# Optimization experiments

Measured on AMD Instinct MI355X. Metric: run time of the kernel, lower is better.

## Reference

```python
import jax, jax.numpy as jnp
import numpy as np

N, D, H, O, E, K = 8192, 1024, 4096, 1024, 8, 3  # tokens, in_dim, hidden, out_dim, experts, topk


def setup_inputs() -> dict:
    key = jax.random.key(0)
    ks = jax.random.split(key, 4)
    s = 0.02
    return {
        "x": jax.random.normal(ks[0], (N, D), jnp.float32),
        "gate_w": jax.random.normal(ks[1], (D, E), jnp.float32) * s,
        "gate_b": jnp.zeros((E,), jnp.float32),
        "w1": jax.random.normal(ks[2], (E, D, H), jnp.float32) * s,
        "b1": jnp.zeros((E, H), jnp.float32),
        "w2": jax.random.normal(ks[3], (E, H, O), jnp.float32) * s,
        "b2": jnp.zeros((E, O), jnp.float32),
    }


def reference(x, gate_w, gate_b, w1, b1, w2, b2):
    # Gate: scores over experts, top-k mask, softmax renormalized over selected experts
    scores = x @ gate_w + gate_b                                   # [N, E]
    _, topk_idx = jax.lax.top_k(scores, K)                         # [N, K]
    mask = jax.nn.one_hot(topk_idx, E, dtype=scores.dtype).sum(1)  # [N, E] (topk indices are distinct)
    weights = jax.nn.softmax(scores, axis=-1) * mask
    weights = weights / (weights.sum(-1, keepdims=True) + 1e-8)
    # Dense all-expert MLP (faithful to original: every expert runs on every token)
    h = jax.nn.relu(jnp.einsum('nd,edh->neh', x, w1) + b1)         # [N, E, H]
    outs = jnp.einsum('neh,eho->neo', h, w2) + b2                  # [N, E, O]
    # Weighted combine over experts
    return jnp.einsum('ne,neo->no', weights, outs)                 # [N, O]
```

## Files before the change

### kernel.cpp

```cpp
#include <hip/hip_runtime.h>
#include <hip/hip_bf16.h>
#include <hip/hip_fp16.h>

#define N_TOK 8192
#define DIM_D 1024
#define DIM_H 4096
#define DIM_O 1024
#define NEXP  8
#define TOPK  3

#define CAP_ROWS  25600
#define MAX_TILES 200
#define NXCD      8
#define MT_PER    (MAX_TILES / NXCD)
#define MT_GRP    5

typedef _Float16 f16_t;
typedef _Float16 f16x4 __attribute__((ext_vector_type(4)));
typedef _Float16 f16x8 __attribute__((ext_vector_type(8)));
typedef float    floatx4 __attribute__((ext_vector_type(4)));

__device__ __forceinline__ void gld_lds16(const void* g, void* l) {
  __builtin_amdgcn_global_load_lds(
      (__attribute__((address_space(1))) void*)(void*)g,
      (__attribute__((address_space(3))) void*)l, 16, 0, 0);
}

__device__ __forceinline__ void decode_tile(int bid, int nbn, int* mt, int* nidx) {
  const int xcd = bid & (NXCD - 1);
  const int lid = bid >> 3;
  const int per = MT_GRP * nbn;
  const int group = lid / per;
  const int rem = lid - group * per;
  const int n = rem / MT_GRP;
  const int g = rem - n * MT_GRP;
  *mt = xcd * MT_PER + group * MT_GRP + g;
  *nidx = n;
}

__global__ __launch_bounds__(256) void gate_kernel(
    const float* __restrict__ x, const float* __restrict__ gw,
    const float* __restrict__ gb, float* __restrict__ wts,
    int* __restrict__ lists, int* __restrict__ cnt) {
  const int token = blockIdx.x * 4 + (threadIdx.x >> 6);
  const int lane = threadIdx.x & 63;
  float s[NEXP];
#pragma unroll
  for (int e = 0; e < NEXP; e++) s[e] = 0.f;
  const float* xr = x + (size_t)token * DIM_D;
  for (int d = lane; d < DIM_D; d += 64) {
    const float xv = xr[d];
    const float* g = gw + (size_t)d * NEXP;
#pragma unroll
    for (int e = 0; e < NEXP; e++) s[e] += xv * g[e];
  }
#pragma unroll
  for (int off = 32; off > 0; off >>= 1) {
#pragma unroll
    for (int e = 0; e < NEXP; e++) s[e] += __shfl_xor(s[e], off, 64);
  }
#pragma unroll
  for (int e = 0; e < NEXP; e++) s[e] += gb[e];

  float mx = s[0];
#pragma unroll
  for (int e = 1; e < NEXP; e++) mx = fmaxf(mx, s[e]);
  float p[NEXP];
  float den = 0.f;
#pragma unroll
  for (int e = 0; e < NEXP; e++) { p[e] = expf(s[e] - mx); den += p[e]; }

  bool sel[NEXP];
#pragma unroll
  for (int e = 0; e < NEXP; e++) sel[e] = false;
  for (int k = 0; k < TOPK; k++) {
    int bj = 0;
    float bv = -1e30f;
#pragma unroll
    for (int e = 0; e < NEXP; e++) {
      if (!sel[e] && s[e] > bv) { bv = s[e]; bj = e; }
    }
    sel[bj] = true;
  }
  float msum = 1e-8f * den;
#pragma unroll
  for (int e = 0; e < NEXP; e++) msum += sel[e] ? p[e] : 0.f;
  const float inv = 1.f / msum;
  if (lane < NEXP) {
    wts[(size_t)token * NEXP + lane] = sel[lane] ? p[lane] * inv : 0.f;
  }
  if (lane == 0) {
#pragma unroll
    for (int e = 0; e < NEXP; e++) {
      if (sel[e]) {
        const int pos = atomicAdd(&cnt[e], 1);
        lists[e * N_TOK + pos] = token;
      }
    }
  }
}

__global__ void plan_kernel(const int* __restrict__ cnt, int* __restrict__ start,
                            int* __restrict__ table, int* __restrict__ total) {
  if (threadIdx.x == 0) {
    int r0 = 0, t = 0;
    for (int e = 0; e < NEXP; e++) {
      start[e] = r0;
      const int nt = (cnt[e] + 127) >> 7;
      for (int i = 0; i < nt; i++) table[t++] = (e << 16) | ((r0 >> 7) + i);
      r0 += nt << 7;
    }
    total[0] = t;
  }
}

__global__ __launch_bounds__(256) void fill_kernel(
    const int* __restrict__ cnt, const int* __restrict__ start,
    const int* __restrict__ lists, const float* __restrict__ wts,
    int* __restrict__ rowtok, float* __restrict__ roww) {
  const int e = blockIdx.y;
  const int i = blockIdx.x * 256 + threadIdx.x;
  const int c = cnt[e];
  const int pad = (c + 127) & ~127;
  if (i >= pad) return;
  const int r = start[e] + i;
  if (i < c) {
    const int t = lists[e * N_TOK + i];
    rowtok[r] = t;
    roww[r] = wts[(size_t)t * NEXP + e];
  } else {
    rowtok[r] = -1;
    roww[r] = 0.f;
  }
}

__global__ __launch_bounds__(256) void cvt_f32_f16(
    const float* __restrict__ in, f16_t* __restrict__ out, int n4) {
  const int i = blockIdx.x * 256 + threadIdx.x;
  if (i >= n4) return;
  const float4 v = ((const float4*)in)[i];
  f16x4 o;
  o.x = (f16_t)v.x; o.y = (f16_t)v.y; o.z = (f16_t)v.z; o.w = (f16_t)v.w;
  ((f16x4*)out)[i] = o;
}

__global__ __launch_bounds__(256) void cvt_transpose(
    const float* __restrict__ in, f16_t* __restrict__ out, int R, int C) {
  __shared__ float tile[32][33];
  const int e = blockIdx.z;
  const int r0 = blockIdx.y * 32, c0 = blockIdx.x * 32;
  const int lc = threadIdx.x & 31, lr0 = threadIdx.x >> 5;
  const float* src = in + (size_t)e * R * C;
#pragma unroll
  for (int i = 0; i < 4; i++) {
    const int rr = lr0 + i * 8;
    tile[rr][lc] = src[(size_t)(r0 + rr) * C + c0 + lc];
  }
  __syncthreads();
  f16_t* dst = out + (size_t)e * C * R;
#pragma unroll
  for (int i = 0; i < 4; i++) {
    const int cc = lr0 + i * 8;
    dst[(size_t)(c0 + cc) * R + r0 + lc] = (f16_t)tile[lc][cc];
  }
}

__global__ __launch_bounds__(256, 2) void gemm1_moe(
    const f16_t* __restrict__ xb, const f16_t* __restrict__ w1t,
    const float* __restrict__ b1, const int* __restrict__ rowtok,
    const int* __restrict__ table, const int* __restrict__ total,
    f16_t* __restrict__ hg, int Hc, int cH, int nbn) {
  int mt, nidx;
  decode_tile(blockIdx.x, nbn, &mt, &nidx);
  if (mt >= total[0]) return;
  const int ent = table[mt];
  const int e = ent >> 16;
  const int r0 = (ent & 0xffff) << 7;
  const int n0 = nidx * 128;

  __shared__ __align__(16) f16_t Asm[128 * 32];
  __shared__ __align__(16) f16_t Bsm[128 * 32];
  const int tid = threadIdx.x;
  const int wave = tid >> 6, lane = tid & 63;
  const int q = lane >> 4, r = lane & 15;
  const int waveM = (wave >> 1) * 64, waveN = (wave & 1) * 64;

  const floatx4 zero = {0.f, 0.f, 0.f, 0.f};
  floatx4 acc[4][4];
#pragma unroll
  for (int mi = 0; mi < 4; mi++)
#pragma unroll
    for (int ni = 0; ni < 4; ni++) acc[mi][ni] = zero;

  const f16_t* BT = w1t + (size_t)e * DIM_H * DIM_D + (size_t)cH * DIM_D;

  const int s0 = tid, s1 = tid + 256;
  const int row0 = s0 >> 2, row1 = s1 >> 2;
  const int gs0 = (s0 & 3) ^ ((row0 >> 1) & 3);
  const int gs1 = (s1 & 3) ^ ((row1 >> 1) & 3);
  const int tok0 = max(rowtok[r0 + row0], 0);
  const int tok1 = max(rowtok[r0 + row1], 0);
  const f16_t* Ar0 = xb + (size_t)tok0 * DIM_D + gs0 * 8;
  const f16_t* Ar1 = xb + (size_t)tok1 * DIM_D + gs1 * 8;
  const f16_t* Br0 = BT + (size_t)(n0 + row0) * DIM_D + gs0 * 8;
  const f16_t* Br1 = BT + (size_t)(n0 + row1) * DIM_D + gs1 * 8;
  f16_t* AsmB0 = &Asm[(wave * 64) * 8];
  f16_t* AsmB1 = &Asm[(256 + wave * 64) * 8];
  f16_t* BsmB0 = &Bsm[(wave * 64) * 8];
  f16_t* BsmB1 = &Bsm[(256 + wave * 64) * 8];

  for (int k0 = 0; k0 < DIM_D; k0 += 32) {
    gld_lds16(Ar0 + k0, AsmB0);
    gld_lds16(Ar1 + k0, AsmB1);
    gld_lds16(Br0 + k0, BsmB0);
    gld_lds16(Br1 + k0, BsmB1);
    __syncthreads();
    f16x8 af[4], bfr[4];
#pragma unroll
    for (int i = 0; i < 4; i++) {
      const int rowa = waveM + i * 16 + r;
      af[i] = *(const f16x8*)&Asm[rowa * 32 + ((q ^ ((rowa >> 1) & 3)) << 3)];
      const int rowb = waveN + i * 16 + r;
      bfr[i] = *(const f16x8*)&Bsm[rowb * 32 + ((q ^ ((rowb >> 1) & 3)) << 3)];
    }
#pragma unroll
    for (int mi = 0; mi < 4; mi++)
#pragma unroll
      for (int ni = 0; ni < 4; ni++)
        acc[mi][ni] = __builtin_amdgcn_mfma_f32_16x16x32_f16(
            af[mi], bfr[ni], acc[mi][ni], 0, 0, 0);
    __syncthreads();
  }

#pragma unroll
  for (int mi = 0; mi < 4; mi++)
#pragma unroll
    for (int ni = 0; ni < 4; ni++) {
      const int gcol = n0 + waveN + ni * 16 + r;
      const float bv = b1[(size_t)e * DIM_H + cH + gcol];
#pragma unroll
      for (int rr = 0; rr < 4; rr++) {
        const int grow = r0 + waveM + mi * 16 + q * 4 + rr;
        hg[(size_t)grow * Hc + gcol] = (f16_t)fmaxf(acc[mi][ni][rr] + bv, 0.f);
      }
    }
}

__global__ __launch_bounds__(256, 2) void gemm2_moe(
    const f16_t* __restrict__ hg, const f16_t* __restrict__ w2t,
    const float* __restrict__ b2, const int* __restrict__ rowtok,
    const float* __restrict__ roww, const int* __restrict__ table,
    const int* __restrict__ total, float* __restrict__ out, int Hc, int cH,
    int addBias) {
  int mt, nidx;
  decode_tile(blockIdx.x, DIM_O / 128, &mt, &nidx);
  if (mt >= total[0]) return;
  const int ent = table[mt];
  const int e = ent >> 16;
  const int r0 = (ent & 0xffff) << 7;
  const int n0 = nidx * 128;

  __shared__ __align__(16) f16_t Asm[128 * 32];
  __shared__ __align__(16) f16_t Bsm[128 * 32];
  const int tid = threadIdx.x;
  const int wave = tid >> 6, lane = tid & 63;
  const int q = lane >> 4, r = lane & 15;
  const int waveM = (wave >> 1) * 64, waveN = (wave & 1) * 64;

  const floatx4 zero = {0.f, 0.f, 0.f, 0.f};
  floatx4 acc[4][4];
#pragma unroll
  for (int mi = 0; mi < 4; mi++)
#pragma unroll
    for (int ni = 0; ni < 4; ni++) acc[mi][ni] = zero;

  const f16_t* BT = w2t + (size_t)e * DIM_O * DIM_H + cH;

  const int s0 = tid, s1 = tid + 256;
  const int row0 = s0 >> 2, row1 = s1 >> 2;
  const int gs0 = (s0 & 3) ^ ((row0 >> 1) & 3);
  const int gs1 = (s1 & 3) ^ ((row1 >> 1) & 3);
  const f16_t* Ar0 = hg + (size_t)(r0 + row0) * Hc + gs0 * 8;
  const f16_t* Ar1 = hg + (size_t)(r0 + row1) * Hc + gs1 * 8;
  const f16_t* Br0 = BT + (size_t)(n0 + row0) * DIM_H + gs0 * 8;
  const f16_t* Br1 = BT + (size_t)(n0 + row1) * DIM_H + gs1 * 8;
  f16_t* AsmB0 = &Asm[(wave * 64) * 8];
  f16_t* AsmB1 = &Asm[(256 + wave * 64) * 8];
  f16_t* BsmB0 = &Bsm[(wave * 64) * 8];
  f16_t* BsmB1 = &Bsm[(256 + wave * 64) * 8];

  for (int k0 = 0; k0 < Hc; k0 += 32) {
    gld_lds16(Ar0 + k0, AsmB0);
    gld_lds16(Ar1 + k0, AsmB1);
    gld_lds16(Br0 + k0, BsmB0);
    gld_lds16(Br1 + k0, BsmB1);
    __syncthreads();
    f16x8 af[4], bfr[4];
#pragma unroll
    for (int i = 0; i < 4; i++) {
      const int rowa = waveM + i * 16 + r;
      af[i] = *(const f16x8*)&Asm[rowa * 32 + ((q ^ ((rowa >> 1) & 3)) << 3)];
      const int rowb = waveN + i * 16 + r;
      bfr[i] = *(const f16x8*)&Bsm[rowb * 32 + ((q ^ ((rowb >> 1) & 3)) << 3)];
    }
#pragma unroll
    for (int mi = 0; mi < 4; mi++)
#pragma unroll
      for (int ni = 0; ni < 4; ni++)
        acc[mi][ni] = __builtin_amdgcn_mfma_f32_16x16x32_f16(
            af[mi], bfr[ni], acc[mi][ni], 0, 0, 0);
    __syncthreads();
  }

#pragma unroll
  for (int mi = 0; mi < 4; mi++)
#pragma unroll
    for (int ni = 0; ni < 4; ni++) {
      const int gcol = n0 + waveN + ni * 16 + r;
      const float bv = addBias ? b2[(size_t)e * DIM_O + gcol] : 0.f;
#pragma unroll
      for (int rr = 0; rr < 4; rr++) {
        const int grow = r0 + waveM + mi * 16 + q * 4 + rr;
        const int t = rowtok[grow];
        if (t >= 0) {
          const float w = roww[grow];
          unsafeAtomicAdd(&out[(size_t)t * DIM_O + gcol],
                          w * (acc[mi][ni][rr] + bv));
        }
      }
    }
}

extern "C" void kernel_launch(void* const* d_in, const int* in_sizes, int n_in,
                              void* d_out, int out_size, void* d_ws, size_t ws_size,
                              hipStream_t stream) {
  const float* x      = (const float*)d_in[0];
  const float* gate_w = (const float*)d_in[1];
  const float* gate_b = (const float*)d_in[2];
  const float* w1     = (const float*)d_in[3];
  const float* b1     = (const float*)d_in[4];
  const float* w2     = (const float*)d_in[5];
  const float* b2     = (const float*)d_in[6];
  float* out = (float*)d_out;

  char* ws = (char*)d_ws;
  const size_t off_wts    = 0;
  const size_t off_lists  = off_wts + 262144;
  const size_t off_cnt    = off_lists + 262144;
  const size_t off_start  = off_cnt + 512;
  const size_t off_total  = off_start + 512;
  const size_t off_table  = off_total + 512;
  const size_t off_rowtok = off_table + 2048;
  const size_t off_roww   = off_rowtok + 102400;
  const size_t META       = 1 << 20;
  const size_t off_w1t = META;
  const size_t off_w2t = off_w1t + (size_t)NEXP * DIM_H * DIM_D * 2;
  const size_t off_xb  = off_w2t + (size_t)NEXP * DIM_O * DIM_H * 2;
  const size_t off_hg  = off_xb + (size_t)N_TOK * DIM_D * 2;

  float* wts   = (float*)(ws + off_wts);
  int*   lists = (int*)(ws + off_lists);
  int*   cnt   = (int*)(ws + off_cnt);
  int*   start = (int*)(ws + off_start);
  int*   total = (int*)(ws + off_total);
  int*   table = (int*)(ws + off_table);
  int*   rowtok= (int*)(ws + off_rowtok);
  float* roww  = (float*)(ws + off_roww);
  f16_t* w1t   = (f16_t*)(ws + off_w1t);
  f16_t* w2t   = (f16_t*)(ws + off_w2t);
  f16_t* xb    = (f16_t*)(ws + off_xb);
  f16_t* hg    = (f16_t*)(ws + off_hg);

  int Hc = 512;
  for (int cand = 4096; cand >= 512; cand >>= 1) {
    if (off_hg + (size_t)CAP_ROWS * cand * 2 <= ws_size) { Hc = cand; break; }
  }
  const int nchunks = DIM_H / Hc;

  hipMemsetAsync(cnt, 0, 512, stream);
  hipMemsetAsync(d_out, 0, (size_t)out_size * sizeof(float), stream);

  gate_kernel<<<N_TOK / 4, 256, 0, stream>>>(x, gate_w, gate_b, wts, lists, cnt);
  plan_kernel<<<1, 64, 0, stream>>>(cnt, start, table, total);
  fill_kernel<<<dim3(N_TOK / 256, NEXP), 256, 0, stream>>>(
      cnt, start, lists, wts, rowtok, roww);

  const int n4 = N_TOK * DIM_D / 4;
  cvt_f32_f16<<<(n4 + 255) / 256, 256, 0, stream>>>(x, xb, n4);
  cvt_transpose<<<dim3(DIM_H / 32, DIM_D / 32, NEXP), 256, 0, stream>>>(
      w1, w1t, DIM_D, DIM_H);
  cvt_transpose<<<dim3(DIM_O / 32, DIM_H / 32, NEXP), 256, 0, stream>>>(
      w2, w2t, DIM_H, DIM_O);

  for (int c = 0; c < nchunks; c++) {
    const int cH = c * Hc;
    const int nbn1 = Hc / 128;
    gemm1_moe<<<dim3(nbn1 * MAX_TILES), 256, 0, stream>>>(
        xb, w1t, b1, rowtok, table, total, hg, Hc, cH, nbn1);
    gemm2_moe<<<dim3((DIM_O / 128) * MAX_TILES), 256, 0, stream>>>(
        hg, w2t, b2, rowtok, roww, table, total, out, Hc, cH, c == 0);
  }
}
```

Before: 1.226 ms.

## Triple-buffer LDS tiles in MoE GEMMs with vmcnt-based async prefetch

Both expert GEMM kernels now keep three LDS stages for A and B, issuing global-to-LDS loads two k-steps ahead. A raw s_waitcnt vmcnt plus s_barrier replaces the two __syncthreads per iteration, so each step waits only for the oldest stage. The goal is to overlap global memory latency with MFMA work and cut barrier count. LDS use triples to 48KB per block, which may reduce occupancy below the launch-bounds target of 2, and the manual waitcnt relies on load ordering being correct.

```diff
diff --git a/kernel.cpp b/kernel.cpp
--- a/kernel.cpp
+++ b/kernel.cpp
@@ -25,6 +25,8 @@
       (__attribute__((address_space(1))) void*)(void*)g,
       (__attribute__((address_space(3))) void*)l, 16, 0, 0);
 }
+
+#define WAITBAR(N) asm volatile("s_waitcnt vmcnt(" #N ")\n\ts_barrier" ::: "memory")
 
 __device__ __forceinline__ void decode_tile(int bid, int nbn, int* mt, int* nidx) {
   const int xcd = bid & (NXCD - 1);
@@ -178,8 +180,8 @@
   const int r0 = (ent & 0xffff) << 7;
   const int n0 = nidx * 128;
 
-  __shared__ __align__(16) f16_t Asm[128 * 32];
-  __shared__ __align__(16) f16_t Bsm[128 * 32];
+  __shared__ __align__(16) f16_t Asm[3][4096];
+  __shared__ __align__(16) f16_t Bsm[3][4096];
   const int tid = threadIdx.x;
   const int wave = tid >> 6, lane = tid & 63;
   const int q = lane >> 4, r = lane & 15;
@@ -204,24 +206,38 @@
   const f16_t* Ar1 = xb + (size_t)tok1 * DIM_D + gs1 * 8;
   const f16_t* Br0 = BT + (size_t)(n0 + row0) * DIM_D + gs0 * 8;
   const f16_t* Br1 = BT + (size_t)(n0 + row1) * DIM_D + gs1 * 8;
-  f16_t* AsmB0 = &Asm[(wave * 64) * 8];
-  f16_t* AsmB1 = &Asm[(256 + wave * 64) * 8];
-  f16_t* BsmB0 = &Bsm[(wave * 64) * 8];
-  f16_t* BsmB1 = &Bsm[(256 + wave * 64) * 8];
-
-  for (int k0 = 0; k0 < DIM_D; k0 += 32) {
-    gld_lds16(Ar0 + k0, AsmB0);
-    gld_lds16(Ar1 + k0, AsmB1);
-    gld_lds16(Br0 + k0, BsmB0);
-    gld_lds16(Br1 + k0, BsmB1);
-    __syncthreads();
+  const int dst0 = (wave * 64) * 8;
+  const int dst1 = (256 + wave * 64) * 8;
+
+  const int nk = DIM_D / 32;
+
+#define STAGE1(b, kk)                          \
+  do {                                         \
+    gld_lds16(Ar0 + (kk) * 32, &Asm[b][dst0]); \
+    gld_lds16(Ar1 + (kk) * 32, &Asm[b][dst1]); \
+    gld_lds16(Br0 + (kk) * 32, &Bsm[b][dst0]); \
+    gld_lds16(Br1 + (kk) * 32, &Bsm[b][dst1]); \
+  } while (0)
+
+  STAGE1(0, 0);
+  STAGE1(1, 1);
+  WAITBAR(4);
+
+  int cur = 0;
+  for (int t = 0; t < nk; ++t) {
+    const bool more = (t + 2) < nk;
+    int stg = cur + 2; if (stg >= 3) stg -= 3;
+    if (more) STAGE1(stg, t + 2);
+
+    const f16_t* Ab = Asm[cur];
+    const f16_t* Bb = Bsm[cur];
     f16x8 af[4], bfr[4];
 #pragma unroll
     for (int i = 0; i < 4; i++) {
       const int rowa = waveM + i * 16 + r;
-      af[i] = *(const f16x8*)&Asm[rowa * 32 + ((q ^ ((rowa >> 1) & 3)) << 3)];
+      af[i] = *(const f16x8*)&Ab[rowa * 32 + ((q ^ ((rowa >> 1) & 3)) << 3)];
       const int rowb = waveN + i * 16 + r;
-      bfr[i] = *(const f16x8*)&Bsm[rowb * 32 + ((q ^ ((rowb >> 1) & 3)) << 3)];
+      bfr[i] = *(const f16x8*)&Bb[rowb * 32 + ((q ^ ((rowb >> 1) & 3)) << 3)];
     }
 #pragma unroll
     for (int mi = 0; mi < 4; mi++)
@@ -229,8 +245,14 @@
       for (int ni = 0; ni < 4; ni++)
         acc[mi][ni] = __builtin_amdgcn_mfma_f32_16x16x32_f16(
             af[mi], bfr[ni], acc[mi][ni], 0, 0, 0);
-    __syncthreads();
-  }
+
+    if (t < nk - 1) {
+      if (more) WAITBAR(4);
+      else      WAITBAR(0);
+    }
+    cur += 1; if (cur >= 3) cur -= 3;
+  }
+#undef STAGE1
 
 #pragma unroll
   for (int mi = 0; mi < 4; mi++)
@@ -260,8 +282,8 @@
   const int r0 = (ent & 0xffff) << 7;
   const int n0 = nidx * 128;
 
-  __shared__ __align__(16) f16_t Asm[128 * 32];
-  __shared__ __align__(16) f16_t Bsm[128 * 32];
+  __shared__ __align__(16) f16_t Asm[3][4096];
+  __shared__ __align__(16) f16_t Bsm[3][4096];
   const int tid = threadIdx.x;
   const int wave = tid >> 6, lane = tid & 63;
   const int q = lane >> 4, r = lane & 15;
@@ -284,24 +306,38 @@
   const f16_t* Ar1 = hg + (size_t)(r0 + row1) * Hc + gs1 * 8;
   const f16_t* Br0 = BT + (size_t)(n0 + row0) * DIM_H + gs0 * 8;
   const f16_t* Br1 = BT + (size_t)(n0 + row1) * DIM_H + gs1 * 8;
-  f16_t* AsmB0 = &Asm[(wave * 64) * 8];
-  f16_t* AsmB1 = &Asm[(256 + wave * 64) * 8];
-  f16_t* BsmB0 = &Bsm[(wave * 64) * 8];
-  f16_t* BsmB1 = &Bsm[(256 + wave * 64) * 8];
-
-  for (int k0 = 0; k0 < Hc; k0 += 32) {
-    gld_lds16(Ar0 + k0, AsmB0);
-    gld_lds16(Ar1 + k0, AsmB1);
-    gld_lds16(Br0 + k0, BsmB0);
-    gld_lds16(Br1 + k0, BsmB1);
-    __syncthreads();
+  const int dst0 = (wave * 64) * 8;
+  const int dst1 = (256 + wave * 64) * 8;
+
+  const int nk = Hc / 32;
+
+#define STAGE2(b, kk)                          \
+  do {                                         \
+    gld_lds16(Ar0 + (kk) * 32, &Asm[b][dst0]); \
+    gld_lds16(Ar1 + (kk) * 32, &Asm[b][dst1]); \
+    gld_lds16(Br0 + (kk) * 32, &Bsm[b][dst0]); \
+    gld_lds16(Br1 + (kk) * 32, &Bsm[b][dst1]); \
+  } while (0)
+
+  STAGE2(0, 0);
+  STAGE2(1, 1);
+  WAITBAR(4);
+
+  int cur = 0;
+  for (int t = 0; t < nk; ++t) {
+    const bool more = (t + 2) < nk;
+    int stg = cur + 2; if (stg >= 3) stg -= 3;
+    if (more) STAGE2(stg, t + 2);
+
+    const f16_t* Ab = Asm[cur];
+    const f16_t* Bb = Bsm[cur];
     f16x8 af[4], bfr[4];
 #pragma unroll
     for (int i = 0; i < 4; i++) {
       const int rowa = waveM + i * 16 + r;
-      af[i] = *(const f16x8*)&Asm[rowa * 32 + ((q ^ ((rowa >> 1) & 3)) << 3)];
+      af[i] = *(const f16x8*)&Ab[rowa * 32 + ((q ^ ((rowa >> 1) & 3)) << 3)];
       const int rowb = waveN + i * 16 + r;
-      bfr[i] = *(const f16x8*)&Bsm[rowb * 32 + ((q ^ ((rowb >> 1) & 3)) << 3)];
+      bfr[i] = *(const f16x8*)&Bb[rowb * 32 + ((q ^ ((rowb >> 1) & 3)) << 3)];
     }
 #pragma unroll
     for (int mi = 0; mi < 4; mi++)
@@ -309,8 +345,14 @@
       for (int ni = 0; ni < 4; ni++)
         acc[mi][ni] = __builtin_amdgcn_mfma_f32_16x16x32_f16(
             af[mi], bfr[ni], acc[mi][ni], 0, 0, 0);
-    __syncthreads();
-  }
+
+    if (t < nk - 1) {
+      if (more) WAITBAR(4);
+      else      WAITBAR(0);
+    }
+    cur += 1; if (cur >= 3) cur -= 3;
+  }
+#undef STAGE2
 
 #pragma unroll
   for (int mi = 0; mi < 4; mi++)
```

New measurement: 1.323 ms. +7.9%, slower.

## Enlarge MoE GEMM tiles to 256x256 with double-buffered LDS and 512 threads

Applied to the files above, without the earlier changes.

Both expert GEMMs move from 128x128 tiles with a single 32-wide K stage to 256x256 tiles with 64-wide K stages, double-buffered in LDS, run by 8 waves per block. The token-row padding and tile table switch to 256-row granularity, and the grouped XCD tile mapping becomes a simple row-major per-XCD mapping. The aim is more reuse per loaded tile and overlap of the next stage's global-to-LDS copy with the current stage's MFMA work. In exchange, the XOR swizzle is dropped, so LDS bank conflicts may appear. The LDS footprint of about 128KB also limits each CU to one block, and the larger padding wastes more rows.

```diff
diff --git a/kernel.cpp b/kernel.cpp
--- a/kernel.cpp
+++ b/kernel.cpp
@@ -9,11 +9,10 @@
 #define NEXP  8
 #define TOPK  3
 
-#define CAP_ROWS  25600
-#define MAX_TILES 200
+#define CAP_ROWS  26624
+#define MAX_TILES 104
 #define NXCD      8
-#define MT_PER    (MAX_TILES / NXCD)
-#define MT_GRP    5
+#define NMT_XCD   (MAX_TILES / NXCD)
 
 typedef _Float16 f16_t;
 typedef _Float16 f16x4 __attribute__((ext_vector_type(4)));
@@ -29,13 +28,9 @@
 __device__ __forceinline__ void decode_tile(int bid, int nbn, int* mt, int* nidx) {
   const int xcd = bid & (NXCD - 1);
   const int lid = bid >> 3;
-  const int per = MT_GRP * nbn;
-  const int group = lid / per;
-  const int rem = lid - group * per;
-  const int n = rem / MT_GRP;
-  const int g = rem - n * MT_GRP;
-  *mt = xcd * MT_PER + group * MT_GRP + g;
-  *nidx = n;
+  const int m_local = lid / nbn;
+  *nidx = lid - m_local * nbn;
+  *mt = xcd * NMT_XCD + m_local;
 }
 
 __global__ __launch_bounds__(256) void gate_kernel(
@@ -106,9 +101,9 @@
     int r0 = 0, t = 0;
     for (int e = 0; e < NEXP; e++) {
       start[e] = r0;
-      const int nt = (cnt[e] + 127) >> 7;
-      for (int i = 0; i < nt; i++) table[t++] = (e << 16) | ((r0 >> 7) + i);
-      r0 += nt << 7;
+      const int nt = (cnt[e] + 255) >> 8;
+      for (int i = 0; i < nt; i++) table[t++] = (e << 16) | ((r0 >> 8) + i);
+      r0 += nt << 8;
     }
     total[0] = t;
   }
@@ -121,7 +116,7 @@
   const int e = blockIdx.y;
   const int i = blockIdx.x * 256 + threadIdx.x;
   const int c = cnt[e];
-  const int pad = (c + 127) & ~127;
+  const int pad = (c + 255) & ~255;
   if (i >= pad) return;
   const int r = start[e] + i;
   if (i < c) {
@@ -165,7 +160,8 @@
   }
 }
 
-__global__ __launch_bounds__(256, 2) void gemm1_moe(
+
+__global__ __launch_bounds__(512, 2) void gemm1_moe(
     const f16_t* __restrict__ xb, const f16_t* __restrict__ w1t,
     const float* __restrict__ b1, const int* __restrict__ rowtok,
     const int* __restrict__ table, const int* __restrict__ total,
@@ -175,152 +171,169 @@
   if (mt >= total[0]) return;
   const int ent = table[mt];
   const int e = ent >> 16;
-  const int r0 = (ent & 0xffff) << 7;
-  const int n0 = nidx * 128;
-
-  __shared__ __align__(16) f16_t Asm[128 * 32];
-  __shared__ __align__(16) f16_t Bsm[128 * 32];
+  const int r0 = (ent & 0xffff) << 8;
+  const int n0 = nidx * 256;
+
+  __shared__ __align__(16) f16_t Asm[2][256 * 64];
+  __shared__ __align__(16) f16_t Bsm[2][256 * 64];
   const int tid = threadIdx.x;
   const int wave = tid >> 6, lane = tid & 63;
   const int q = lane >> 4, r = lane & 15;
-  const int waveM = (wave >> 1) * 64, waveN = (wave & 1) * 64;
+  const int wr = wave >> 2, wc = wave & 3;
+  const int wrM = wr * 128, wcN = wc * 64;
 
   const floatx4 zero = {0.f, 0.f, 0.f, 0.f};
-  floatx4 acc[4][4];
-#pragma unroll
-  for (int mi = 0; mi < 4; mi++)
+  floatx4 acc[8][4];
+#pragma unroll
+  for (int mi = 0; mi < 8; mi++)
 #pragma unroll
     for (int ni = 0; ni < 4; ni++) acc[mi][ni] = zero;
 
   const f16_t* BT = w1t + (size_t)e * DIM_H * DIM_D + (size_t)cH * DIM_D;
 
-  const int s0 = tid, s1 = tid + 256;
-  const int row0 = s0 >> 2, row1 = s1 >> 2;
-  const int gs0 = (s0 & 3) ^ ((row0 >> 1) & 3);
-  const int gs1 = (s1 & 3) ^ ((row1 >> 1) & 3);
-  const int tok0 = max(rowtok[r0 + row0], 0);
-  const int tok1 = max(rowtok[r0 + row1], 0);
-  const f16_t* Ar0 = xb + (size_t)tok0 * DIM_D + gs0 * 8;
-  const f16_t* Ar1 = xb + (size_t)tok1 * DIM_D + gs1 * 8;
-  const f16_t* Br0 = BT + (size_t)(n0 + row0) * DIM_D + gs0 * 8;
-  const f16_t* Br1 = BT + (size_t)(n0 + row1) * DIM_D + gs1 * 8;
-  f16_t* AsmB0 = &Asm[(wave * 64) * 8];
-  f16_t* AsmB1 = &Asm[(256 + wave * 64) * 8];
-  f16_t* BsmB0 = &Bsm[(wave * 64) * 8];
-  f16_t* BsmB1 = &Bsm[(256 + wave * 64) * 8];
-
-  for (int k0 = 0; k0 < DIM_D; k0 += 32) {
-    gld_lds16(Ar0 + k0, AsmB0);
-    gld_lds16(Ar1 + k0, AsmB1);
-    gld_lds16(Br0 + k0, BsmB0);
-    gld_lds16(Br1 + k0, BsmB1);
+  const int slot = lane & 7;
+  const f16_t* aptr[4];
+  const f16_t* bptr[4];
+#pragma unroll
+  for (int j = 0; j < 4; j++) {
+    const int row = j * 64 + wave * 8 + (lane >> 3);
+    const int tok = max(rowtok[r0 + row], 0);
+    aptr[j] = xb + (size_t)tok * DIM_D + slot * 8;
+    bptr[j] = BT + (size_t)(n0 + row) * DIM_D + slot * 8;
+  }
+#define STAGE1(b, kt)                                               \
+  do {                                                              \
+    _Pragma("unroll")                                               \
+    for (int j = 0; j < 4; j++) {                                   \
+      gld_lds16(aptr[j] + (kt) * 64, &Asm[b][j * 4096 + wave * 512]); \
+      gld_lds16(bptr[j] + (kt) * 64, &Bsm[b][j * 4096 + wave * 512]); \
+    }                                                               \
+  } while (0)
+
+  const int nk = DIM_D / 64;
+  STAGE1(0, 0);
+  int buf = 0;
+  for (int t = 0; t < nk; ++t) {
     __syncthreads();
-    f16x8 af[4], bfr[4];
-#pragma unroll
-    for (int i = 0; i < 4; i++) {
-      const int rowa = waveM + i * 16 + r;
-      af[i] = *(const f16x8*)&Asm[rowa * 32 + ((q ^ ((rowa >> 1) & 3)) << 3)];
-      const int rowb = waveN + i * 16 + r;
-      bfr[i] = *(const f16x8*)&Bsm[rowb * 32 + ((q ^ ((rowb >> 1) & 3)) << 3)];
-    }
-#pragma unroll
-    for (int mi = 0; mi < 4; mi++)
+    if (t + 1 < nk) STAGE1(buf ^ 1, t + 1);
+#pragma unroll
+    for (int kk = 0; kk < 2; kk++) {
+      f16x8 af[8], bf[4];
+#pragma unroll
+      for (int mi = 0; mi < 8; mi++)
+        af[mi] = *(const f16x8*)&Asm[buf][(wrM + mi * 16 + r) * 64 + kk * 32 + q * 8];
 #pragma unroll
       for (int ni = 0; ni < 4; ni++)
-        acc[mi][ni] = __builtin_amdgcn_mfma_f32_16x16x32_f16(
-            af[mi], bfr[ni], acc[mi][ni], 0, 0, 0);
-    __syncthreads();
-  }
-
-#pragma unroll
-  for (int mi = 0; mi < 4; mi++)
+        bf[ni] = *(const f16x8*)&Bsm[buf][(wcN + ni * 16 + r) * 64 + kk * 32 + q * 8];
+#pragma unroll
+      for (int mi = 0; mi < 8; mi++)
+#pragma unroll
+        for (int ni = 0; ni < 4; ni++)
+          acc[mi][ni] = __builtin_amdgcn_mfma_f32_16x16x32_f16(
+              af[mi], bf[ni], acc[mi][ni], 0, 0, 0);
+    }
+    buf ^= 1;
+  }
+#undef STAGE1
+
+#pragma unroll
+  for (int mi = 0; mi < 8; mi++)
 #pragma unroll
     for (int ni = 0; ni < 4; ni++) {
-      const int gcol = n0 + waveN + ni * 16 + r;
+      const int gcol = n0 + wcN + ni * 16 + r;
       const float bv = b1[(size_t)e * DIM_H + cH + gcol];
 #pragma unroll
       for (int rr = 0; rr < 4; rr++) {
-        const int grow = r0 + waveM + mi * 16 + q * 4 + rr;
+        const int grow = r0 + wrM + mi * 16 + q * 4 + rr;
         hg[(size_t)grow * Hc + gcol] = (f16_t)fmaxf(acc[mi][ni][rr] + bv, 0.f);
       }
     }
 }
 
-__global__ __launch_bounds__(256, 2) void gemm2_moe(
+__global__ __launch_bounds__(512, 2) void gemm2_moe(
     const f16_t* __restrict__ hg, const f16_t* __restrict__ w2t,
     const float* __restrict__ b2, const int* __restrict__ rowtok,
     const float* __restrict__ roww, const int* __restrict__ table,
     const int* __restrict__ total, float* __restrict__ out, int Hc, int cH,
     int addBias) {
   int mt, nidx;
-  decode_tile(blockIdx.x, DIM_O / 128, &mt, &nidx);
+  decode_tile(blockIdx.x, DIM_O / 256, &mt, &nidx);
   if (mt >= total[0]) return;
   const int ent = table[mt];
   const int e = ent >> 16;
-  const int r0 = (ent & 0xffff) << 7;
-  const int n0 = nidx * 128;
-
-  __shared__ __align__(16) f16_t Asm[128 * 32];
-  __shared__ __align__(16) f16_t Bsm[128 * 32];
+  const int r0 = (ent & 0xffff) << 8;
+  const int n0 = nidx * 256;
+
+  __shared__ __align__(16) f16_t Asm[2][256 * 64];
+  __shared__ __align__(16) f16_t Bsm[2][256 * 64];
   const int tid = threadIdx.x;
   const int wave = tid >> 6, lane = tid & 63;
   const int q = lane >> 4, r = lane & 15;
-  const int waveM = (wave >> 1) * 64, waveN = (wave & 1) * 64;
+  const int wr = wave >> 2, wc = wave & 3;
+  const int wrM = wr * 128, wcN = wc * 64;
 
   const floatx4 zero = {0.f, 0.f, 0.f, 0.f};
-  floatx4 acc[4][4];
-#pragma unroll
-  for (int mi = 0; mi < 4; mi++)
+  floatx4 acc[8][4];
+#pragma unroll
+  for (int mi = 0; mi < 8; mi++)
 #pragma unroll
     for (int ni = 0; ni < 4; ni++) acc[mi][ni] = zero;
 
   const f16_t* BT = w2t + (size_t)e * DIM_O * DIM_H + cH;
 
-  const int s0 = tid, s1 = tid + 256;
-  const int row0 = s0 >> 2, row1 = s1 >> 2;
-  const int gs0 = (s0 & 3) ^ ((row0 >> 1) & 3);
-  const int gs1 = (s1 & 3) ^ ((row1 >> 1) & 3);
-  const f16_t* Ar0 = hg + (size_t)(r0 + row0) * Hc + gs0 * 8;
-  const f16_t* Ar1 = hg + (size_t)(r0 + row1) * Hc + gs1 * 8;
-  const f16_t* Br0 = BT + (size_t)(n0 + row0) * DIM_H + gs0 * 8;
-  const f16_t* Br1 = BT + (size_t)(n0 + row1) * DIM_H + gs1 * 8;
-  f16_t* AsmB0 = &Asm[(wave * 64) * 8];
-  f16_t* AsmB1 = &Asm[(256 + wave * 64) * 8];
-  f16_t* BsmB0 = &Bsm[(wave * 64) * 8];
-  f16_t* BsmB1 = &Bsm[(256 + wave * 64) * 8];
-
-  for (int k0 = 0; k0 < Hc; k0 += 32) {
-    gld_lds16(Ar0 + k0, AsmB0);
-    gld_lds16(Ar1 + k0, AsmB1);
-    gld_lds16(Br0 + k0, BsmB0);
-    gld_lds16(Br1 + k0, BsmB1);
+  const int slot = lane & 7;
+  const f16_t* aptr[4];
+  const f16_t* bptr[4];
+#pragma unroll
+  for (int j = 0; j < 4; j++) {
+    const int row = j * 64 + wave * 8 + (lane >> 3);
+    aptr[j] = hg + (size_t)(r0 + row) * Hc + slot * 8;
+    bptr[j] = BT + (size_t)(n0 + row) * DIM_H + slot * 8;
+  }
+#define STAGE2(b, kt)                                               \
+  do {                                                              \
+    _Pragma("unroll")                                               \
+    for (int j = 0; j < 4; j++) {                                   \
+      gld_lds16(aptr[j] + (kt) * 64, &Asm[b][j * 4096 + wave * 512]); \
+      gld_lds16(bptr[j] + (kt) * 64, &Bsm[b][j * 4096 + wave * 512]); \
+    }                                                               \
+  } while (0)
+
+  const int nk = Hc / 64;
+  STAGE2(0, 0);
+  int buf = 0;
+  for (int t = 0; t < nk; ++t) {
     __syncthreads();
-    f16x8 af[4], bfr[4];
-#pragma unroll
-    for (int i = 0; i < 4; i++) {
-      const int rowa = waveM + i * 16 + r;
-      af[i] = *(const f16x8*)&Asm[rowa * 32 + ((q ^ ((rowa >> 1) & 3)) << 3)];
-      const int rowb = waveN + i * 16 + r;
-      bfr[i] = *(const f16x8*)&Bsm[rowb * 32 + ((q ^ ((rowb >> 1) & 3)) << 3)];
-    }
-#pragma unroll
-    for (int mi = 0; mi < 4; mi++)
+    if (t + 1 < nk) STAGE2(buf ^ 1, t + 1);
+#pragma unroll
+    for (int kk = 0; kk < 2; kk++) {
+      f16x8 af[8], bf[4];
+#pragma unroll
+      for (int mi = 0; mi < 8; mi++)
+        af[mi] = *(const f16x8*)&Asm[buf][(wrM + mi * 16 + r) * 64 + kk * 32 + q * 8];
 #pragma unroll
       for (int ni = 0; ni < 4; ni++)
-        acc[mi][ni] = __builtin_amdgcn_mfma_f32_16x16x32_f16(
-            af[mi], bfr[ni], acc[mi][ni], 0, 0, 0);
-    __syncthreads();
-  }
-
-#pragma unroll
-  for (int mi = 0; mi < 4; mi++)
+        bf[ni] = *(const f16x8*)&Bsm[buf][(wcN + ni * 16 + r) * 64 + kk * 32 + q * 8];
+#pragma unroll
+      for (int mi = 0; mi < 8; mi++)
+#pragma unroll
+        for (int ni = 0; ni < 4; ni++)
+          acc[mi][ni] = __builtin_amdgcn_mfma_f32_16x16x32_f16(
+              af[mi], bf[ni], acc[mi][ni], 0, 0, 0);
+    }
+    buf ^= 1;
+  }
+#undef STAGE2
+
+#pragma unroll
+  for (int mi = 0; mi < 8; mi++)
 #pragma unroll
     for (int ni = 0; ni < 4; ni++) {
-      const int gcol = n0 + waveN + ni * 16 + r;
+      const int gcol = n0 + wcN + ni * 16 + r;
       const float bv = addBias ? b2[(size_t)e * DIM_O + gcol] : 0.f;
 #pragma unroll
       for (int rr = 0; rr < 4; rr++) {
-        const int grow = r0 + waveM + mi * 16 + q * 4 + rr;
+        const int grow = r0 + wrM + mi * 16 + q * 4 + rr;
         const int t = rowtok[grow];
         if (t >= 0) {
           const float w = roww[grow];
@@ -351,7 +364,7 @@
   const size_t off_total  = off_start + 512;
   const size_t off_table  = off_total + 512;
   const size_t off_rowtok = off_table + 2048;
-  const size_t off_roww   = off_rowtok + 102400;
+  const size_t off_roww   = off_rowtok + 114688;
   const size_t META       = 1 << 20;
   const size_t off_w1t = META;
   const size_t off_w2t = off_w1t + (size_t)NEXP * DIM_H * DIM_D * 2;
@@ -394,10 +407,10 @@
 
   for (int c = 0; c < nchunks; c++) {
     const int cH = c * Hc;
-    const int nbn1 = Hc / 128;
-    gemm1_moe<<<dim3(nbn1 * MAX_TILES), 256, 0, stream>>>(
+    const int nbn1 = Hc / 256;
+    gemm1_moe<<<dim3(MAX_TILES * nbn1), 512, 0, stream>>>(
         xb, w1t, b1, rowtok, table, total, hg, Hc, cH, nbn1);
-    gemm2_moe<<<dim3((DIM_O / 128) * MAX_TILES), 256, 0, stream>>>(
+    gemm2_moe<<<dim3(MAX_TILES * (DIM_O / 256)), 512, 0, stream>>>(
         hg, w2t, b2, rowtok, roww, table, total, out, Hc, cH, c == 0);
   }
 }
```

After: 1.515 ms. +23.6%, slower.

## Replace atomic scatter-add in expert GEMM2 with fp16 staging and gather combine

Applied to the files above, without the earlier changes.

GEMM2 now writes per-row expert outputs in fp16 to a staging buffer instead of doing weighted float atomic adds into the output. A new combine kernel uses a token-to-row map built in the fill step to gather each token's three expert rows, weight them and write (or accumulate) the output, so the output memset is no longer needed. This removes atomic contention but adds an extra staging write/read pass per H chunk and rounds expert outputs to fp16 before combining, and the staging buffer may force a smaller H chunk.

```diff
diff --git a/kernel.cpp b/kernel.cpp
--- a/kernel.cpp
+++ b/kernel.cpp
@@ -90,11 +90,13 @@
     wts[(size_t)token * NEXP + lane] = sel[lane] ? p[lane] * inv : 0.f;
   }
   if (lane == 0) {
+    int kk = 0;
 #pragma unroll
     for (int e = 0; e < NEXP; e++) {
       if (sel[e]) {
         const int pos = atomicAdd(&cnt[e], 1);
-        lists[e * N_TOK + pos] = token;
+        lists[e * N_TOK + pos] = token | (kk << 14);
+        kk++;
       }
     }
   }
@@ -117,7 +119,8 @@
 __global__ __launch_bounds__(256) void fill_kernel(
     const int* __restrict__ cnt, const int* __restrict__ start,
     const int* __restrict__ lists, const float* __restrict__ wts,
-    int* __restrict__ rowtok, float* __restrict__ roww) {
+    int* __restrict__ rowtok, float* __restrict__ roww,
+    int* __restrict__ tok2row) {
   const int e = blockIdx.y;
   const int i = blockIdx.x * 256 + threadIdx.x;
   const int c = cnt[e];
@@ -125,9 +128,12 @@
   if (i >= pad) return;
   const int r = start[e] + i;
   if (i < c) {
-    const int t = lists[e * N_TOK + i];
+    const int v = lists[e * N_TOK + i];
+    const int t = v & 0x3FFF;
+    const int k = v >> 14;
     rowtok[r] = t;
     roww[r] = wts[(size_t)t * NEXP + e];
+    tok2row[t * 4 + k] = r;
   } else {
     rowtok[r] = -1;
     roww[r] = 0.f;
@@ -248,9 +254,8 @@
 
 __global__ __launch_bounds__(256, 2) void gemm2_moe(
     const f16_t* __restrict__ hg, const f16_t* __restrict__ w2t,
-    const float* __restrict__ b2, const int* __restrict__ rowtok,
-    const float* __restrict__ roww, const int* __restrict__ table,
-    const int* __restrict__ total, float* __restrict__ out, int Hc, int cH,
+    const float* __restrict__ b2, const int* __restrict__ table,
+    const int* __restrict__ total, f16_t* __restrict__ og, int Hc, int cH,
     int addBias) {
   int mt, nidx;
   decode_tile(blockIdx.x, DIM_O / 128, &mt, &nidx);
@@ -321,14 +326,34 @@
 #pragma unroll
       for (int rr = 0; rr < 4; rr++) {
         const int grow = r0 + waveM + mi * 16 + q * 4 + rr;
-        const int t = rowtok[grow];
-        if (t >= 0) {
-          const float w = roww[grow];
-          unsafeAtomicAdd(&out[(size_t)t * DIM_O + gcol],
-                          w * (acc[mi][ni][rr] + bv));
-        }
+        og[(size_t)grow * DIM_O + gcol] = (f16_t)(acc[mi][ni][rr] + bv);
       }
     }
+}
+
+__global__ __launch_bounds__(256) void combine_kernel(
+    const f16_t* __restrict__ og, const float* __restrict__ roww,
+    const int* __restrict__ tok2row, float* __restrict__ out, int first) {
+  const int t = blockIdx.x;
+  const int c0 = threadIdx.x * 4;
+  const int ra = tok2row[t * 4 + 0];
+  const int rb = tok2row[t * 4 + 1];
+  const int rc = tok2row[t * 4 + 2];
+  const float wa = roww[ra], wb = roww[rb], wc = roww[rc];
+  const f16x4 a = *(const f16x4*)&og[(size_t)ra * DIM_O + c0];
+  const f16x4 b = *(const f16x4*)&og[(size_t)rb * DIM_O + c0];
+  const f16x4 c = *(const f16x4*)&og[(size_t)rc * DIM_O + c0];
+  float4 o;
+  o.x = wa * (float)a.x + wb * (float)b.x + wc * (float)c.x;
+  o.y = wa * (float)a.y + wb * (float)b.y + wc * (float)c.y;
+  o.z = wa * (float)a.z + wb * (float)b.z + wc * (float)c.z;
+  o.w = wa * (float)a.w + wb * (float)b.w + wc * (float)c.w;
+  float4* op = (float4*)&out[(size_t)t * DIM_O + c0];
+  if (!first) {
+    const float4 p = *op;
+    o.x += p.x; o.y += p.y; o.z += p.z; o.w += p.w;
+  }
+  *op = o;
 }
 
 extern "C" void kernel_launch(void* const* d_in, const int* in_sizes, int n_in,
@@ -344,46 +369,49 @@
   float* out = (float*)d_out;
 
   char* ws = (char*)d_ws;
-  const size_t off_wts    = 0;
-  const size_t off_lists  = off_wts + 262144;
-  const size_t off_cnt    = off_lists + 262144;
-  const size_t off_start  = off_cnt + 512;
-  const size_t off_total  = off_start + 512;
-  const size_t off_table  = off_total + 512;
-  const size_t off_rowtok = off_table + 2048;
-  const size_t off_roww   = off_rowtok + 102400;
-  const size_t META       = 1 << 20;
+  const size_t off_wts     = 0;
+  const size_t off_lists   = off_wts + 262144;
+  const size_t off_cnt     = off_lists + 262144;
+  const size_t off_start   = off_cnt + 512;
+  const size_t off_total   = off_start + 512;
+  const size_t off_table   = off_total + 512;
+  const size_t off_rowtok  = off_table + 2048;
+  const size_t off_roww    = off_rowtok + 102400;
+  const size_t off_tok2row = off_roww + 102400;
+  const size_t META        = 1 << 20;
   const size_t off_w1t = META;
   const size_t off_w2t = off_w1t + (size_t)NEXP * DIM_H * DIM_D * 2;
   const size_t off_xb  = off_w2t + (size_t)NEXP * DIM_O * DIM_H * 2;
   const size_t off_hg  = off_xb + (size_t)N_TOK * DIM_D * 2;
-
-  float* wts   = (float*)(ws + off_wts);
-  int*   lists = (int*)(ws + off_lists);
-  int*   cnt   = (int*)(ws + off_cnt);
-  int*   start = (int*)(ws + off_start);
-  int*   total = (int*)(ws + off_total);
-  int*   table = (int*)(ws + off_table);
-  int*   rowtok= (int*)(ws + off_rowtok);
-  float* roww  = (float*)(ws + off_roww);
-  f16_t* w1t   = (f16_t*)(ws + off_w1t);
-  f16_t* w2t   = (f16_t*)(ws + off_w2t);
-  f16_t* xb    = (f16_t*)(ws + off_xb);
-  f16_t* hg    = (f16_t*)(ws + off_hg);
+  const size_t og_sz   = (size_t)CAP_ROWS * DIM_O * 2;
+
+  float* wts    = (float*)(ws + off_wts);
+  int*   lists  = (int*)(ws + off_lists);
+  int*   cnt    = (int*)(ws + off_cnt);
+  int*   start  = (int*)(ws + off_start);
+  int*   total  = (int*)(ws + off_total);
+  int*   table  = (int*)(ws + off_table);
+  int*   rowtok = (int*)(ws + off_rowtok);
+  float* roww   = (float*)(ws + off_roww);
+  int*   tok2row= (int*)(ws + off_tok2row);
+  f16_t* w1t    = (f16_t*)(ws + off_w1t);
+  f16_t* w2t    = (f16_t*)(ws + off_w2t);
+  f16_t* xb     = (f16_t*)(ws + off_xb);
+  f16_t* hg     = (f16_t*)(ws + off_hg);
 
   int Hc = 512;
   for (int cand = 4096; cand >= 512; cand >>= 1) {
-    if (off_hg + (size_t)CAP_ROWS * cand * 2 <= ws_size) { Hc = cand; break; }
+    if (off_hg + (size_t)CAP_ROWS * cand * 2 + og_sz <= ws_size) { Hc = cand; break; }
   }
   const int nchunks = DIM_H / Hc;
+  f16_t* og = (f16_t*)(ws + off_hg + (size_t)CAP_ROWS * Hc * 2);
 
   hipMemsetAsync(cnt, 0, 512, stream);
-  hipMemsetAsync(d_out, 0, (size_t)out_size * sizeof(float), stream);
 
   gate_kernel<<<N_TOK / 4, 256, 0, stream>>>(x, gate_w, gate_b, wts, lists, cnt);
   plan_kernel<<<1, 64, 0, stream>>>(cnt, start, table, total);
   fill_kernel<<<dim3(N_TOK / 256, NEXP), 256, 0, stream>>>(
-      cnt, start, lists, wts, rowtok, roww);
+      cnt, start, lists, wts, rowtok, roww, tok2row);
 
   const int n4 = N_TOK * DIM_D / 4;
   cvt_f32_f16<<<(n4 + 255) / 256, 256, 0, stream>>>(x, xb, n4);
@@ -398,6 +426,7 @@
     gemm1_moe<<<dim3(nbn1 * MAX_TILES), 256, 0, stream>>>(
         xb, w1t, b1, rowtok, table, total, hg, Hc, cH, nbn1);
     gemm2_moe<<<dim3((DIM_O / 128) * MAX_TILES), 256, 0, stream>>>(
-        hg, w2t, b2, rowtok, roww, table, total, out, Hc, cH, c == 0);
-  }
-}
+        hg, w2t, b2, table, total, og, Hc, cH, c == 0);
+    combine_kernel<<<N_TOK, 256, 0, stream>>>(og, roww, tok2row, out, c == 0);
+  }
+}
```

Result: faster. 1.170 ms (-4.5%).
